# Optimization experiments

Hardware: AMD Instinct MI355X
Metric: run time of the kernel (lower is better)

## Reference

```python
import jax, jax.numpy as jnp
import numpy as np

K = 8          # kernels per group
G = 64         # num groups
DIVISOR = 2    # min(2, g)
H = G // DIVISOR  # 32 groups per diff branch
KLEN = 9       # conv kernel taps
N = 256
L = 2048


def _dilations(input_length):
    max_exp = int(np.log2((input_length - 1) / (KLEN - 1)))
    d = (2 ** np.arange(max_exp + 1)).astype(np.int64)
    p = ((KLEN - 1) * d) // 2
    return d, p


def setup_inputs() -> dict:
    key = jax.random.key(0)
    kx, kw = jax.random.split(key)
    X = jax.random.normal(kx, (N, 1, L), dtype=jnp.float32)
    num_dil = len(_dilations(L)[0])  # 8 for L=2048
    W = jax.random.normal(kw, (num_dil, DIVISOR, K * H, 1, KLEN), dtype=jnp.float32)
    W = W - W.mean(-1, keepdims=True)
    W = W / jnp.abs(W).sum(-1, keepdims=True)
    return {"X": X, "W": W}


def _conv1d(x, w, d, p):
    # x: [N, 1, T], w: [O, 1, 9] -> [N, O, T_out]
    return jax.lax.conv_general_dilated(
        x, w, window_strides=(1,), padding=[(p, p)], rhs_dilation=(d,),
        dimension_numbers=("NCH", "OIH", "NCH"))


def _safe_sqrt_clamp(z):
    # forward-identical to clamp(min=0).sqrt(); grad-safe at z<=0
    zs = jnp.where(z > 0, z, 1.0)
    return jnp.where(z > 0, jnp.sqrt(zs), 0.0)


def reference(X, W):
    num_examples = X.shape[0]
    dilations, paddings = _dilations(X.shape[-1])
    diff_X = jnp.diff(X, axis=-1)  # [N, 1, L-1]
    n_idx = jnp.arange(num_examples)[:, None, None]
    h_idx = jnp.arange(H)[None, :, None]
    feats = []
    for di in range(len(dilations)):
        d, p = int(dilations[di]), int(paddings[di])
        for diff_index in range(DIVISOR):
            inp = X if diff_index == 0 else diff_X
            _Z = _conv1d(inp, W[di, diff_index], d, p)              # [N, K*H, T]
            _Z = _Z.reshape(num_examples, H, K, -1)                 # [N, H, K, T]
            max_values = _Z.max(axis=2)                             # [N, H, T]
            max_indices = jnp.argmax(_Z, axis=2)
            min_indices = jnp.argmin(_Z, axis=2)
            count_max = jnp.zeros((num_examples, H, K), X.dtype).at[
                n_idx, h_idx, max_indices].add(max_values)
            count_min = jnp.zeros((num_examples, H, K), X.dtype).at[
                n_idx, h_idx, min_indices].add(jnp.ones_like(max_values))
            feats.append(count_max)
            feats.append(count_min)
    Zout = jnp.concatenate(feats, axis=1).reshape(num_examples, -1)  # [N, num_features]
    return _safe_sqrt_clamp(Zout)
```

## Files before the change

kernel.cpp:

```cpp
#include <hip/hip_runtime.h>
#include <math.h>

namespace {

typedef short short8 __attribute__((ext_vector_type(8)));
typedef float f32x16 __attribute__((ext_vector_type(16)));
typedef unsigned int u32;

constexpr int NEX = 256, LLEN = 2048, FEATS = 8192;
constexpr int PL = 512;
constexpr int XSZ = 4096;

__device__ __forceinline__ u32 bfsplit(float x) {
  u32 b = __float_as_uint(x);
  u32 hb = (b + 0x7fffu + ((b >> 16) & 1u)) >> 16;
  float lo = x - __uint_as_float(hb << 16);
  u32 b2 = __float_as_uint(lo);
  u32 lb = (b2 + 0x7fffu + ((b2 >> 16) & 1u)) >> 16;
  return hb | (lb << 16);
}

__device__ __forceinline__ float max8(const float* v, int o) {
  float m0 = fmaxf(fmaxf(v[o+0], v[o+1]), v[o+2]);
  float m1 = fmaxf(fmaxf(v[o+3], v[o+4]), v[o+5]);
  float m2 = fmaxf(v[o+6], v[o+7]);
  return fmaxf(fmaxf(m0, m1), m2);
}
__device__ __forceinline__ float min8(const float* v, int o) {
  float m0 = fminf(fminf(v[o+0], v[o+1]), v[o+2]);
  float m1 = fminf(fminf(v[o+3], v[o+4]), v[o+5]);
  float m2 = fminf(v[o+6], v[o+7]);
  return fminf(fminf(m0, m1), m2);
}

#define MFMA __builtin_amdgcn_mfma_f32_32x32x16_bf16

template<int D, int DI>
__device__ __forceinline__ void body(
    const float* __restrict__ X, const float* __restrict__ W,
    float* __restrict__ out, u32* __restrict__ xhl,
    float* __restrict__ binsM, float* __restrict__ binsN,
    float* __restrict__ fin)
{
  const int n = blockIdx.x, diff = blockIdx.y, tid = threadIdx.x;
  const int lane = tid & 63, wave = tid >> 6;
  const int col = lane & 31, hi = lane >> 5;

  const float* xr = X + n * LLEN;
  for (int i = tid; i < XSZ; i += 256) {
    float x = 0.f;
    if (diff) { if (i >= PL && i < PL + LLEN - 1) x = xr[i - PL + 1] - xr[i - PL]; }
    else      { if (i >= PL && i < PL + LLEN)     x = xr[i - PL]; }
    xhl[i] = bfsplit(x);
  }

  float* myM = binsM + wave * 1024 + lane;
  float* myN = binsN + wave * 1024 + lane;
  #pragma unroll
  for (int b = 0; b < 16; ++b) { myM[b * 64] = 0.f; myN[b * 64] = 0.f; }
  __syncthreads();

  const float* wall = W + (DI * 2 + diff) * (256 * 9);

  const int g_of_r = ((col >> 4) << 1) | ((col >> 2) & 1);
  const int k_of_r = (col & 3) | (((col >> 3) & 1) << 2);
  const int kloc = g_of_r * 8 + k_of_r;

  const f32x16 czero = {};

  for (int kt2 = 0; kt2 < 2; ++kt2) {
    short8 ah, al;
    {
      const float* wrow = wall + (wave * 64 + kt2 * 32 + kloc) * 9;
      #pragma unroll
      for (int e = 0; e < 8; ++e) {
        int j = hi * 8 + e;
        float wv = (j < 9) ? wrow[j] : 0.f;
        u32 p = bfsplit(wv);
        ah[e] = (short)(p & 0xffffu);
        al[e] = (short)(p >> 16);
      }
    }

    #pragma clang loop unroll_count(1)
    for (int tt = 0; tt < 64; ++tt) {
      const int ebase = PL + tt * 32 + col + (hi * 8 - 4) * D;
      u32 uu[8];
      #pragma unroll
      for (int e = 0; e < 8; ++e) uu[e] = xhl[ebase + e * D];
      union { short8 s; u32 u[4]; } bh, bl;
      #pragma unroll
      for (int p = 0; p < 4; ++p) {
        bh.u[p] = __builtin_amdgcn_perm(uu[2*p+1], uu[2*p], 0x05040100u);
        bl.u[p] = __builtin_amdgcn_perm(uu[2*p+1], uu[2*p], 0x07060302u);
      }

      f32x16 c;
      c = MFMA(al, bh.s, czero, 0, 0, 0);
      c = MFMA(ah, bl.s, c,     0, 0, 0);
      c = MFMA(ah, bh.s, c,     0, 0, 0);

      float cf[16];
      #pragma unroll
      for (int i = 0; i < 16; ++i)
        cf[i] = __uint_as_float((__float_as_uint(c[i]) & 0xFFFFFFF0u) |
                                (u32)(i & 7));

      const float zx0 = max8(cf, 0), zn0 = min8(cf, 0);
      const float zx1 = max8(cf, 8), zn1 = min8(cf, 8);
      const u32 kx0 = __float_as_uint(zx0) & 7u;
      const u32 kn0 = __float_as_uint(zn0) & 7u;
      const u32 kx1 = __float_as_uint(zx1) & 7u;
      const u32 kn1 = __float_as_uint(zn1) & 7u;

      myM[kx0 * 64]       += zx0;
      myM[(8 + kx1) * 64] += zx1;
      myN[kn0 * 64]       += 1.f;
      myN[(8 + kn1) * 64] += 1.f;
    }

    {
      const int s = lane & 31;
      const int hi_s = (s >> 3) & 1;
      const int b = ((s >> 4) << 3) | (s & 7);
      const float* src =
          (lane < 32 ? binsM : binsN) + wave * 1024 + b * 64 + 32 * hi_s;
      float acc = 0.f;
      #pragma unroll
      for (int c2 = 0; c2 < 32; ++c2) acc += src[c2];
      fin[((wave * 32 + s) * 2 + kt2) * 2 + (lane >= 32 ? 1 : 0)] = acc;
    }

    if (kt2 == 0) {
      #pragma unroll
      for (int b = 0; b < 16; ++b) { myM[b * 64] = 0.f; myN[b * 64] = 0.f; }
    }
  }
  __syncthreads();

  const int w2 = tid >> 6, kt2f = (tid >> 5) & 1, r = tid & 31;
  float M = fin[((w2 * 32 + r) * 2 + kt2f) * 2 + 0];
  float N = fin[((w2 * 32 + r) * 2 + kt2f) * 2 + 1];

  if (diff) {
    const float* wrow = wall + tid * 9;
    float z = 0.f;
    #pragma unroll
    for (int j = 0; j < 9; ++j) {
      u32 u = xhl[PL + (LLEN - 1) + (j - 4) * D];
      float xh = __uint_as_float((u & 0xffffu) << 16);
      float xl = __uint_as_float((u >> 16) << 16);
      u32 wp = bfsplit(wrow[j]);
      float wh = __uint_as_float((wp & 0xffffu) << 16);
      float wl = __uint_as_float((wp >> 16) << 16);
      z += wh * xh + wh * xl + wl * xh;
    }
    float* zrow = binsM;
    zrow[tid] = z;
    __syncthreads();
    const int h8 = tid & ~7;
    float zxv = zrow[h8], znv = zrow[h8];
    #pragma unroll
    for (int j = 1; j < 8; ++j) {
      zxv = fmaxf(zxv, zrow[h8 + j]);
      znv = fminf(znv, zrow[h8 + j]);
    }
    M -= (z == zxv) ? z : 0.f;
    N -= (z == znv) ? 1.f : 0.f;
  }

  const int base = n * FEATS + (DI * 4 + diff * 2) * 256 + tid;
  out[base]       = M > 0.f ? sqrtf(M) : 0.f;
  out[base + 256] = N > 0.f ? sqrtf(N) : 0.f;
}

__global__ __launch_bounds__(256, 3) void hydra_kernel(
    const float* __restrict__ X, const float* __restrict__ W,
    float* __restrict__ out)
{
  __shared__ u32   xhl[XSZ];
  __shared__ float binsM[4 * 16 * 64];
  __shared__ float binsN[4 * 16 * 64];
  __shared__ float fin[1024];
  switch (blockIdx.z) {
    case 0: body<1,   0>(X, W, out, xhl, binsM, binsN, fin); break;
    case 1: body<2,   1>(X, W, out, xhl, binsM, binsN, fin); break;
    case 2: body<4,   2>(X, W, out, xhl, binsM, binsN, fin); break;
    case 3: body<8,   3>(X, W, out, xhl, binsM, binsN, fin); break;
    case 4: body<16,  4>(X, W, out, xhl, binsM, binsN, fin); break;
    case 5: body<32,  5>(X, W, out, xhl, binsM, binsN, fin); break;
    case 6: body<64,  6>(X, W, out, xhl, binsM, binsN, fin); break;
    case 7: body<128, 7>(X, W, out, xhl, binsM, binsN, fin); break;
  }
}

}

extern "C" void kernel_launch(void* const* d_in, const int* in_sizes, int n_in,
                              void* d_out, int out_size, void* d_ws, size_t ws_size,
                              hipStream_t stream) {
  const float* X = (const float*)d_in[0];
  const float* W = (const float*)d_in[1];
  float* out = (float*)d_out;
  dim3 grid(NEX, 2, 8);
  hipLaunchKernelGGL(hydra_kernel, grid, dim3(256), 0, stream, X, W, out);
}
```

Measured before the change: 304.8 us.

## Fuse kernel-tile passes, reuse B operands, pack min counts in registers

The two passes over the sequence (one per 32-kernel tile) are merged into a single time loop. Each step's B operand, built from shared memory and permuted into bf16 hi/lo halves, now feeds both weight tiles instead of being rebuilt per tile. Argmin counts move from shared-memory bins to packed 8-bit counters in 64-bit registers, which removes half of the LDS read-modify-write traffic per step. Bin reductions use rotated indices to reduce bank conflicts. The cost is extra register pressure from holding both weight fragments plus the counters, which could lower occupancy under the 3-blocks launch bound. Each 8-bit counter holds at most 64 increments, so it cannot overflow.

```diff
diff --git a/kernel.cpp b/kernel.cpp
--- a/kernel.cpp
+++ b/kernel.cpp
@@ -6,6 +6,7 @@
 typedef short short8 __attribute__((ext_vector_type(8)));
 typedef float f32x16 __attribute__((ext_vector_type(16)));
 typedef unsigned int u32;
+typedef unsigned long long u64;
 
 constexpr int NEX = 256, LLEN = 2048, FEATS = 8192;
 constexpr int PL = 512;
@@ -39,8 +40,7 @@
 __device__ __forceinline__ void body(
     const float* __restrict__ X, const float* __restrict__ W,
     float* __restrict__ out, u32* __restrict__ xhl,
-    float* __restrict__ binsM, float* __restrict__ binsN,
-    float* __restrict__ fin)
+    float* __restrict__ binsM, float* __restrict__ fin)
 {
   const int n = blockIdx.x, diff = blockIdx.y, tid = threadIdx.x;
   const int lane = tid & 63, wave = tid >> 6;
@@ -54,10 +54,9 @@
     xhl[i] = bfsplit(x);
   }
 
-  float* myM = binsM + wave * 1024 + lane;
-  float* myN = binsN + wave * 1024 + lane;
+  float* myM = binsM + wave * 2048 + lane;
   #pragma unroll
-  for (int b = 0; b < 16; ++b) { myM[b * 64] = 0.f; myN[b * 64] = 0.f; }
+  for (int b = 0; b < 32; ++b) myM[b * 64] = 0.f;
   __syncthreads();
 
   const float* wall = W + (DI * 2 + diff) * (256 * 9);
@@ -66,81 +65,112 @@
   const int k_of_r = (col & 3) | (((col >> 3) & 1) << 2);
   const int kloc = g_of_r * 8 + k_of_r;
 
+  short8 ah0, al0, ah1, al1;
+  {
+    const float* w0 = wall + (wave * 64 + kloc) * 9;
+    const float* w1 = w0 + 288;
+    #pragma unroll
+    for (int e = 0; e < 8; ++e) {
+      int j = hi * 8 + e;
+      float v0 = (j < 9) ? w0[j] : 0.f;
+      float v1 = (j < 9) ? w1[j] : 0.f;
+      u32 p0 = bfsplit(v0), p1 = bfsplit(v1);
+      ah0[e] = (short)(p0 & 0xffffu); al0[e] = (short)(p0 >> 16);
+      ah1[e] = (short)(p1 & 0xffffu); al1[e] = (short)(p1 >> 16);
+    }
+  }
+
   const f32x16 czero = {};
-
-  for (int kt2 = 0; kt2 < 2; ++kt2) {
-    short8 ah, al;
+  u64 n00 = 0ull, n01 = 0ull, n10 = 0ull, n11 = 0ull;
+
+  #pragma clang loop unroll_count(1)
+  for (int tt = 0; tt < 64; ++tt) {
+    const int ebase = PL + tt * 32 + col + (hi * 8 - 4) * D;
+    u32 uu[8];
+    #pragma unroll
+    for (int p = 0; p < 4; ++p) {
+      const u32* bp = xhl + (ebase + p * 2 * D);
+      uu[2*p]   = bp[0];
+      uu[2*p+1] = bp[D];
+    }
+    union { short8 s; u32 u[4]; } bh, bl;
+    #pragma unroll
+    for (int p = 0; p < 4; ++p) {
+      bh.u[p] = __builtin_amdgcn_perm(uu[2*p+1], uu[2*p], 0x05040100u);
+      bl.u[p] = __builtin_amdgcn_perm(uu[2*p+1], uu[2*p], 0x07060302u);
+    }
+
     {
-      const float* wrow = wall + (wave * 64 + kt2 * 32 + kloc) * 9;
-      #pragma unroll
-      for (int e = 0; e < 8; ++e) {
-        int j = hi * 8 + e;
-        float wv = (j < 9) ? wrow[j] : 0.f;
-        u32 p = bfsplit(wv);
-        ah[e] = (short)(p & 0xffffu);
-        al[e] = (short)(p >> 16);
-      }
-    }
-
-    #pragma clang loop unroll_count(1)
-    for (int tt = 0; tt < 64; ++tt) {
-      const int ebase = PL + tt * 32 + col + (hi * 8 - 4) * D;
-      u32 uu[8];
-      #pragma unroll
-      for (int e = 0; e < 8; ++e) uu[e] = xhl[ebase + e * D];
-      union { short8 s; u32 u[4]; } bh, bl;
-      #pragma unroll
-      for (int p = 0; p < 4; ++p) {
-        bh.u[p] = __builtin_amdgcn_perm(uu[2*p+1], uu[2*p], 0x05040100u);
-        bl.u[p] = __builtin_amdgcn_perm(uu[2*p+1], uu[2*p], 0x07060302u);
-      }
-
       f32x16 c;
-      c = MFMA(al, bh.s, czero, 0, 0, 0);
-      c = MFMA(ah, bl.s, c,     0, 0, 0);
-      c = MFMA(ah, bh.s, c,     0, 0, 0);
-
+      c = MFMA(al0, bh.s, czero, 0, 0, 0);
+      c = MFMA(ah0, bl.s, c,     0, 0, 0);
+      c = MFMA(ah0, bh.s, c,     0, 0, 0);
       float cf[16];
       #pragma unroll
       for (int i = 0; i < 16; ++i)
         cf[i] = __uint_as_float((__float_as_uint(c[i]) & 0xFFFFFFF0u) |
                                 (u32)(i & 7));
-
       const float zx0 = max8(cf, 0), zn0 = min8(cf, 0);
       const float zx1 = max8(cf, 8), zn1 = min8(cf, 8);
-      const u32 kx0 = __float_as_uint(zx0) & 7u;
-      const u32 kn0 = __float_as_uint(zn0) & 7u;
-      const u32 kx1 = __float_as_uint(zx1) & 7u;
-      const u32 kn1 = __float_as_uint(zn1) & 7u;
-
-      myM[kx0 * 64]       += zx0;
-      myM[(8 + kx1) * 64] += zx1;
-      myN[kn0 * 64]       += 1.f;
-      myN[(8 + kn1) * 64] += 1.f;
-    }
-
+      myM[(__float_as_uint(zx0) & 7u) * 64]       += zx0;
+      myM[(8u + (__float_as_uint(zx1) & 7u)) * 64] += zx1;
+      n00 += 1ull << ((__float_as_uint(zn0) & 7u) * 8u);
+      n01 += 1ull << ((__float_as_uint(zn1) & 7u) * 8u);
+    }
     {
-      const int s = lane & 31;
-      const int hi_s = (s >> 3) & 1;
-      const int b = ((s >> 4) << 3) | (s & 7);
-      const float* src =
-          (lane < 32 ? binsM : binsN) + wave * 1024 + b * 64 + 32 * hi_s;
-      float acc = 0.f;
+      f32x16 c;
+      c = MFMA(al1, bh.s, czero, 0, 0, 0);
+      c = MFMA(ah1, bl.s, c,     0, 0, 0);
+      c = MFMA(ah1, bh.s, c,     0, 0, 0);
+      float cf[16];
       #pragma unroll
-      for (int c2 = 0; c2 < 32; ++c2) acc += src[c2];
-      fin[((wave * 32 + s) * 2 + kt2) * 2 + (lane >= 32 ? 1 : 0)] = acc;
-    }
-
-    if (kt2 == 0) {
-      #pragma unroll
-      for (int b = 0; b < 16; ++b) { myM[b * 64] = 0.f; myN[b * 64] = 0.f; }
-    }
+      for (int i = 0; i < 16; ++i)
+        cf[i] = __uint_as_float((__float_as_uint(c[i]) & 0xFFFFFFF0u) |
+                                (u32)(i & 7));
+      const float zx0 = max8(cf, 0), zn0 = min8(cf, 0);
+      const float zx1 = max8(cf, 8), zn1 = min8(cf, 8);
+      myM[(16u + (__float_as_uint(zx0) & 7u)) * 64] += zx0;
+      myM[(24u + (__float_as_uint(zx1) & 7u)) * 64] += zx1;
+      n10 += 1ull << ((__float_as_uint(zn0) & 7u) * 8u);
+      n11 += 1ull << ((__float_as_uint(zn1) & 7u) * 8u);
+    }
+  }
+
+  const int kt2f = lane >> 5;
+  const int s = lane & 31;
+  const int hi_s = (s >> 3) & 1;
+  const int chunk = s >> 4;
+  const int kk = s & 7;
+  float accM = 0.f;
+  {
+    const int b = kt2f * 16 + chunk * 8 + kk;
+    const float* src = binsM + wave * 2048 + b * 64 + 32 * hi_s;
+    #pragma unroll
+    for (int c2 = 0; c2 < 32; ++c2) accM += src[(c2 + s) & 31];
   }
   __syncthreads();
 
-  const int w2 = tid >> 6, kt2f = (tid >> 5) & 1, r = tid & 31;
-  float M = fin[((w2 * 32 + r) * 2 + kt2f) * 2 + 0];
-  float N = fin[((w2 * 32 + r) * 2 + kt2f) * 2 + 1];
+  u32* nwp = (u32*)(binsM + wave * 2048);
+  nwp[0 * 64 + lane] = (u32)n00; nwp[1 * 64 + lane] = (u32)(n00 >> 32);
+  nwp[2 * 64 + lane] = (u32)n01; nwp[3 * 64 + lane] = (u32)(n01 >> 32);
+  nwp[4 * 64 + lane] = (u32)n10; nwp[5 * 64 + lane] = (u32)(n10 >> 32);
+  nwp[6 * 64 + lane] = (u32)n11; nwp[7 * 64 + lane] = (u32)(n11 >> 32);
+  float accN;
+  {
+    const int w2 = kt2f * 4 + chunk * 2 + (kk >> 2);
+    const u32 sh = (u32)(kk & 3) * 8u;
+    const u32* srcn = nwp + w2 * 64 + 32 * hi_s;
+    u32 a = 0;
+    #pragma unroll
+    for (int c2 = 0; c2 < 32; ++c2)
+      a += (srcn[(c2 + s) & 31] >> sh) & 255u;
+    accN = (float)a;
+  }
+  *(float2*)(fin + (wave * 64 + lane) * 2) = make_float2(accM, accN);
+  __syncthreads();
+
+  float2 mn2 = *(const float2*)(fin + tid * 2);
+  float M = mn2.x, N = mn2.y;
 
   if (diff) {
     const float* wrow = wall + tid * 9;
@@ -179,18 +209,17 @@
     float* __restrict__ out)
 {
   __shared__ u32   xhl[XSZ];
-  __shared__ float binsM[4 * 16 * 64];
-  __shared__ float binsN[4 * 16 * 64];
-  __shared__ float fin[1024];
+  __shared__ float binsM[4 * 32 * 64];
+  __shared__ float fin[512];
   switch (blockIdx.z) {
-    case 0: body<1,   0>(X, W, out, xhl, binsM, binsN, fin); break;
-    case 1: body<2,   1>(X, W, out, xhl, binsM, binsN, fin); break;
-    case 2: body<4,   2>(X, W, out, xhl, binsM, binsN, fin); break;
-    case 3: body<8,   3>(X, W, out, xhl, binsM, binsN, fin); break;
-    case 4: body<16,  4>(X, W, out, xhl, binsM, binsN, fin); break;
-    case 5: body<32,  5>(X, W, out, xhl, binsM, binsN, fin); break;
-    case 6: body<64,  6>(X, W, out, xhl, binsM, binsN, fin); break;
-    case 7: body<128, 7>(X, W, out, xhl, binsM, binsN, fin); break;
+    case 0: body<1,   0>(X, W, out, xhl, binsM, fin); break;
+    case 1: body<2,   1>(X, W, out, xhl, binsM, fin); break;
+    case 2: body<4,   2>(X, W, out, xhl, binsM, fin); break;
+    case 3: body<8,   3>(X, W, out, xhl, binsM, fin); break;
+    case 4: body<16,  4>(X, W, out, xhl, binsM, fin); break;
+    case 5: body<32,  5>(X, W, out, xhl, binsM, fin); break;
+    case 6: body<64,  6>(X, W, out, xhl, binsM, fin); break;
+    case 7: body<128, 7>(X, W, out, xhl, binsM, fin); break;
   }
 }
 
```

After: 267.0 us. 12.4% less time.
